# Optimization experiments

Hardware: AMD Instinct MI355X
Metric: run time of the kernel (lower is better)

Reference implementation:

```python
import jax, jax.numpy as jnp
import numpy as np
from jax import lax

IN_CH = 256
NF = 128
B, H, W = 8, 256, 256


def _bn_relu(y, s, b):
    # inference-mode BatchNorm folded into per-channel affine, then ReLU
    return jax.nn.relu(y * s[None, :, None, None] + b[None, :, None, None])


def _upsample_bilinear_ac(x, scale):
    # bilinear upsample, align_corners=True (matches torch nn.Upsample)
    b, c, h, w = x.shape
    Ho, Wo = h * scale, w * scale
    ys = jnp.arange(Ho, dtype=x.dtype) * ((h - 1) / (Ho - 1))
    xs = jnp.arange(Wo, dtype=x.dtype) * ((w - 1) / (Wo - 1))
    y0 = jnp.floor(ys).astype(jnp.int32)
    x0 = jnp.floor(xs).astype(jnp.int32)
    y1 = jnp.minimum(y0 + 1, h - 1)
    x1 = jnp.minimum(x0 + 1, w - 1)
    wy = (ys - y0.astype(x.dtype))[None, None, :, None]
    wx = (xs - x0.astype(x.dtype))[None, None, None, :]
    # interpolate rows then columns
    top = x[:, :, y0, :] * (1 - wy) + x[:, :, y1, :] * wy      # [b,c,Ho,w]
    out = top[:, :, :, x0] * (1 - wx) + top[:, :, :, x1] * wx  # [b,c,Ho,Wo]
    return out


def setup_inputs() -> dict:
    key = jax.random.key(0)
    ks = jax.random.split(key, 6)
    inp = {
        "x": jax.random.normal(ks[0], (B, 64, H, W), dtype=jnp.float32),
        "w1": jax.random.normal(ks[1], (IN_CH, 64, 8, 8), dtype=jnp.float32) * 0.02,
        "bn1_s": jnp.ones((IN_CH,), jnp.float32),
        "bn1_b": jnp.zeros((IN_CH,), jnp.float32),
        "w_fai": jax.random.normal(ks[2], (NF, IN_CH), dtype=jnp.float32) * 0.05,
        "bnf_s": jnp.ones((NF,), jnp.float32),
        "bnf_b": jnp.zeros((NF,), jnp.float32),
        "w_sit": jax.random.normal(ks[3], (NF, IN_CH), dtype=jnp.float32) * 0.05,
        "bns_s": jnp.ones((NF,), jnp.float32),
        "bns_b": jnp.zeros((NF,), jnp.float32),
        "w_gama": jax.random.normal(ks[4], (NF, IN_CH), dtype=jnp.float32) * 0.05,
        "bng_s": jnp.ones((NF,), jnp.float32),
        "bng_b": jnp.zeros((NF,), jnp.float32),
    }
    return inp


def reference(x, w1, bn1_s, bn1_b, w_fai, bnf_s, bnf_b, w_sit, bns_s, bns_b,
              w_gama, bng_s, bng_b):
    # conv1: 8x8 stride-8 conv, BN, ReLU  -> [B, IN_CH, h, w]
    y = lax.conv_general_dilated(x, w1, window_strides=(8, 8), padding="VALID",
                                 dimension_numbers=("NCHW", "OIHW", "NCHW"))
    y = _bn_relu(y, bn1_s, bn1_b)
    b, c, h, w = y.shape
    n = h * w
    # 1x1 conv projections (einsum), BN, ReLU
    fai = _bn_relu(jnp.einsum("bchw,oc->bohw", y, w_fai), bnf_s, bnf_b)
    sit = _bn_relu(jnp.einsum("bchw,oc->bohw", y, w_sit), bns_s, bns_b)
    gama = _bn_relu(jnp.einsum("bchw,oc->bohw", y, w_gama), bng_s, bng_b)
    fai = fai.reshape(b, NF, n)
    sit = sit.reshape(b, NF, n)
    gama = gama.reshape(b, NF, n)
    # non-local attention: sigmoid(fai^T sit) @ gama^T
    sf = jax.nn.sigmoid(jnp.einsum("bcn,bcm->bnm", fai, sit))  # [b, n, n]
    out = jnp.einsum("bnm,bcm->bcn", sf, gama)                  # [b, NF, n]
    out = out.reshape(b, NF, h, w)
    return _upsample_bilinear_ac(out, 8)
```

## Files before the change

### kernel.cpp

```cpp
#include <hip/hip_runtime.h>

typedef __attribute__((ext_vector_type(8))) short short8_t;
typedef __attribute__((ext_vector_type(4))) float float4_t;

__device__ __forceinline__ unsigned short f2bf(float f) {
    unsigned int u = __float_as_uint(f);
    return (unsigned short)((u + 0x7FFFu + ((u >> 16) & 1u)) >> 16);
}
__device__ __forceinline__ unsigned int pkbf(float a, float b) {
    return (unsigned int)f2bf(a) | ((unsigned int)f2bf(b) << 16);
}

__global__ __launch_bounds__(256) void k_wprep(
    const float* __restrict__ w1, unsigned short* __restrict__ w1s)
{
    const int id = blockIdx.x * 256 + threadIdx.x;
    const float4* s = (const float4*)(w1 + id * 8);
    float4 a = s[0], b = s[1];
    int4 o;
    o.x = pkbf(a.x, a.y); o.y = pkbf(a.z, a.w);
    o.z = pkbf(b.x, b.y); o.w = pkbf(b.z, b.w);
    *(int4*)(w1s + id * 8) = o;
}

__global__ __launch_bounds__(512, 2) void k_conv1(
    const float* __restrict__ x, const unsigned short* __restrict__ w1s,
    float* __restrict__ part)
{
    __shared__ unsigned short At[128 * 40];
    __shared__ unsigned short Bt[256 * 40];
    const int tid = threadIdx.x;
    const int mt = blockIdx.x, kc = blockIdx.y;
    const int m0 = mt * 128;
    const int bi = mt >> 3;
    const int oh0 = (mt & 7) * 4;
    const int lane = tid & 63, wid = tid >> 6;
    const int wm = wid & 1, wn = wid >> 1;
    const int quad = lane >> 4, r16 = lane & 15;
    const bool isA = tid < 256;
    const int tA = tid & 255;
    const int rA = tA >> 4, segA = tA & 15;
    const int ohl = rA >> 2, khl = rA & 3;
    const int rowA = ohl * 32 + segA * 2;
    const int koffA = (khl ^ (segA & 3)) * 8;
    const int kbase = kc * 1024;
    float4_t acc[4][4] = {};
    float4 ra[4];
    int4 rb[4];

    if (isA) {
        const int ic = kbase >> 6, kh0 = (kbase >> 3) & 7;
        const int xr = (oh0 + ohl) * 8 + kh0 + khl;
        const float4* s4 = (const float4*)(x + (((bi * 64 + ic) * 256 + xr) * 256 + segA * 16));
        ra[0] = s4[0]; ra[1] = s4[1]; ra[2] = s4[2]; ra[3] = s4[3];
    } else {
        #pragma unroll
        for (int l = 0; l < 4; ++l) {
            const int slot = l * 256 + tA;
            const int row = slot >> 2, p = slot & 3;
            rb[l] = *(const int4*)(w1s + row * 4096 + kbase + p * 8);
        }
    }

    for (int it = 0; it < 32; ++it) {
        if (isA) {
            int4 p0, p1;
            p0.x = pkbf(ra[0].x, ra[0].y); p0.y = pkbf(ra[0].z, ra[0].w);
            p0.z = pkbf(ra[1].x, ra[1].y); p0.w = pkbf(ra[1].z, ra[1].w);
            p1.x = pkbf(ra[2].x, ra[2].y); p1.y = pkbf(ra[2].z, ra[2].w);
            p1.z = pkbf(ra[3].x, ra[3].y); p1.w = pkbf(ra[3].z, ra[3].w);
            *(int4*)&At[rowA * 40 + koffA] = p0;
            *(int4*)&At[(rowA + 1) * 40 + koffA] = p1;
        } else {
            #pragma unroll
            for (int l = 0; l < 4; ++l) {
                const int slot = l * 256 + tA;
                const int row = slot >> 2, p = slot & 3;
                *(int4*)&Bt[row * 40 + p * 8] = rb[l];
            }
        }
        __syncthreads();
        if (it + 1 < 32) {
            const int k0 = kbase + (it + 1) * 32;
            if (isA) {
                const int ic = k0 >> 6, kh0 = (k0 >> 3) & 7;
                const int xr = (oh0 + ohl) * 8 + kh0 + khl;
                const float4* s4 = (const float4*)(x + (((bi * 64 + ic) * 256 + xr) * 256 + segA * 16));
                ra[0] = s4[0]; ra[1] = s4[1]; ra[2] = s4[2]; ra[3] = s4[3];
            } else {
                #pragma unroll
                for (int l = 0; l < 4; ++l) {
                    const int slot = l * 256 + tA;
                    const int row = slot >> 2, p = slot & 3;
                    rb[l] = *(const int4*)(w1s + row * 4096 + k0 + p * 8);
                }
            }
        }
        short8_t aF[4], bF[4];
        #pragma unroll
        for (int i = 0; i < 4; ++i) {
            const int R = wm * 64 + i * 16 + r16;
            aF[i] = *(const short8_t*)&At[R * 40 + (quad ^ ((r16 >> 1) & 3)) * 8];
        }
        #pragma unroll
        for (int j = 0; j < 4; ++j)
            bF[j] = *(const short8_t*)&Bt[(wn * 64 + j * 16 + r16) * 40 + quad * 8];
        #pragma unroll
        for (int i = 0; i < 4; ++i)
            #pragma unroll
            for (int j = 0; j < 4; ++j)
                acc[i][j] = __builtin_amdgcn_mfma_f32_16x16x32_bf16(aF[i], bF[j], acc[i][j], 0, 0, 0);
        __syncthreads();
    }
    float* pp = part + ((size_t)kc << 21);
    #pragma unroll
    for (int i = 0; i < 4; ++i) {
        const int mg = m0 + wm * 64 + i * 16 + quad * 4;
        #pragma unroll
        for (int j = 0; j < 4; ++j) {
            const int ng = wn * 64 + j * 16 + r16;
            #pragma unroll
            for (int r = 0; r < 4; ++r)
                pp[(mg + r) * 256 + ng] = acc[i][j][r];
        }
    }
}

__global__ __launch_bounds__(256, 4) void k_reduce(
    const float* __restrict__ part, const float* __restrict__ s1,
    const float* __restrict__ b1, unsigned short* __restrict__ y)
{
    const int id = blockIdx.x * 256 + threadIdx.x;
    const int c4 = id & 63;
    const float4* p = (const float4*)part + id;
    float4 a = p[0], b = p[524288], c = p[1048576], d = p[1572864];
    float4 s = ((const float4*)s1)[c4], bb = ((const float4*)b1)[c4];
    float vx = fmaxf((a.x + b.x + c.x + d.x) * s.x + bb.x, 0.f);
    float vy = fmaxf((a.y + b.y + c.y + d.y) * s.y + bb.y, 0.f);
    float vz = fmaxf((a.z + b.z + c.z + d.z) * s.z + bb.z, 0.f);
    float vw = fmaxf((a.w + b.w + c.w + d.w) * s.w + bb.w, 0.f);
    int2 o; o.x = pkbf(vx, vy); o.y = pkbf(vz, vw);
    ((int2*)y)[id] = o;
}

__global__ __launch_bounds__(256, 2) void k_proj3(
    const unsigned short* __restrict__ y,
    const float* __restrict__ w_fai, const float* __restrict__ w_sit,
    const float* __restrict__ w_gama,
    const float* __restrict__ fs, const float* __restrict__ fb,
    const float* __restrict__ ss, const float* __restrict__ sb,
    const float* __restrict__ gs, const float* __restrict__ gb,
    unsigned short* __restrict__ P, unsigned short* __restrict__ G)
{
    __shared__ unsigned short At[64 * 40];
    __shared__ unsigned short Bt[64 * 40];
    const int tid = threadIdx.x;
    const int nt = blockIdx.x, mt = blockIdx.y;
    const int m0 = mt * 64;
    const float *W, *S, *Bb;
    if (nt < 2)      { W = w_fai;  S = fs; Bb = fb; }
    else if (nt < 4) { W = w_sit;  S = ss; Bb = sb; }
    else             { W = w_gama; S = gs; Bb = gb; }
    const int roff = (nt * 64) & 127;
    const int lane = tid & 63, wid = tid >> 6;
    const int wm = wid & 1, wn = wid >> 1;
    const int quad = lane >> 4, r16 = lane & 15;
    float4_t acc[2][2] = {};

    for (int k0 = 0; k0 < 256; k0 += 32) {
        {
            const int row = tid >> 2, pp = tid & 3;
            *(int4*)&At[row * 40 + pp * 8] =
                *(const int4*)(y + (m0 + row) * 256 + k0 + pp * 8);
        }
        #pragma unroll
        for (int l = 0; l < 2; ++l) {
            const int slot = l * 256 + tid;
            const int row = slot >> 3, pp = slot & 7;
            float4 v = *(const float4*)(W + (roff + row) * 256 + k0 + pp * 4);
            int2 wv; wv.x = pkbf(v.x, v.y); wv.y = pkbf(v.z, v.w);
            *(int2*)&Bt[row * 40 + pp * 4] = wv;
        }
        __syncthreads();
        short8_t aF[2], bF[2];
        #pragma unroll
        for (int i = 0; i < 2; ++i)
            aF[i] = *(const short8_t*)&At[(wm * 32 + i * 16 + r16) * 40 + quad * 8];
        #pragma unroll
        for (int j = 0; j < 2; ++j)
            bF[j] = *(const short8_t*)&Bt[(wn * 32 + j * 16 + r16) * 40 + quad * 8];
        #pragma unroll
        for (int i = 0; i < 2; ++i)
            #pragma unroll
            for (int j = 0; j < 2; ++j)
                acc[i][j] = __builtin_amdgcn_mfma_f32_16x16x32_bf16(aF[i], bF[j], acc[i][j], 0, 0, 0);
        __syncthreads();
    }
    #pragma unroll
    for (int i = 0; i < 2; ++i) {
        const int mg = m0 + wm * 32 + i * 16 + quad * 4;
        #pragma unroll
        for (int j = 0; j < 2; ++j) {
            const int nl = wn * 32 + j * 16 + r16;
            const float sc = S[roff + nl], bc = Bb[roff + nl];
            if (nt < 4) {
                const int col = nt * 64 + nl;
                #pragma unroll
                for (int r = 0; r < 4; ++r) {
                    float v = fmaxf(acc[i][j][r] * sc + bc, 0.f);
                    P[(mg + r) * 256 + col] = f2bf(v);
                }
            } else {
                const int c = roff + nl;
                #pragma unroll
                for (int r = 0; r < 4; ++r) {
                    float v = fmaxf(acc[i][j][r] * sc + bc, 0.f);
                    const int sp = mg + r;
                    G[((sp >> 10) * 128 + c) * 1024 + (sp & 1023)] = f2bf(v);
                }
            }
        }
    }
}

#define LSTR 152
__global__ __launch_bounds__(256, 2) void k_attn(
    const unsigned short* __restrict__ P, const unsigned short* __restrict__ G,
    float* __restrict__ Opart)
{
    __shared__ unsigned short At[64 * LSTR];
    __shared__ unsigned short Bt[128 * LSTR];
    __shared__ unsigned short Sl[64 * LSTR];
    const int tid = threadIdx.x;
    const int nt = blockIdx.x, zz = blockIdx.y;
    const int b = zz >> 2, kc = zz & 3;
    const int n0 = nt * 64;
    const int base = b * 1024;
    const int lane = tid & 63, wid = tid >> 6;
    const int wm = wid & 1, wn = wid >> 1;
    const int quad = lane >> 4, r16 = lane & 15;
    float4_t acc2[2][4] = {};

    #pragma unroll
    for (int l = 0; l < 4; ++l) {
        const int slot = l * 256 + tid;
        const int row = slot >> 4, p = slot & 15;
        *(int4*)&At[row * LSTR + p * 8] =
            *(const int4*)(P + (base + n0 + row) * 256 + p * 8);
    }
    for (int ms = 0; ms < 2; ++ms) {
        const int m1 = kc * 256 + ms * 128;
        #pragma unroll
        for (int l = 0; l < 8; ++l) {
            const int slot = l * 256 + tid;
            const int row = slot >> 4, p = slot & 15;
            *(int4*)&Bt[row * LSTR + p * 8] =
                *(const int4*)(P + (base + m1 + row) * 256 + 128 + p * 8);
        }
        __syncthreads();
        float4_t acc1[2][4] = {};
        #pragma unroll
        for (int c = 0; c < 4; ++c) {
            short8_t aF[2], bF[4];
            #pragma unroll
            for (int i = 0; i < 2; ++i)
                aF[i] = *(const short8_t*)&At[(wm * 32 + i * 16 + r16) * LSTR + c * 32 + quad * 8];
            #pragma unroll
            for (int j = 0; j < 4; ++j)
                bF[j] = *(const short8_t*)&Bt[(wn * 64 + j * 16 + r16) * LSTR + c * 32 + quad * 8];
            #pragma unroll
            for (int i = 0; i < 2; ++i)
                #pragma unroll
                for (int j = 0; j < 4; ++j)
                    acc1[i][j] = __builtin_amdgcn_mfma_f32_16x16x32_bf16(aF[i], bF[j], acc1[i][j], 0, 0, 0);
        }
        __syncthreads();
        #pragma unroll
        for (int i = 0; i < 2; ++i) {
            const int nl = wm * 32 + i * 16 + quad * 4;
            #pragma unroll
            for (int j = 0; j < 4; ++j) {
                const int ml = wn * 64 + j * 16 + r16;
                #pragma unroll
                for (int r = 0; r < 4; ++r) {
                    const float xv = acc1[i][j][r];
                    const float e = __expf(-xv);
                    const float v = __builtin_amdgcn_rcpf(1.0f + e);
                    Sl[(nl + r) * LSTR + ml] = f2bf(v);
                }
            }
        }
        #pragma unroll
        for (int l = 0; l < 8; ++l) {
            const int slot = l * 256 + tid;
            const int row = slot >> 4, p = slot & 15;
            *(int4*)&Bt[row * LSTR + p * 8] =
                *(const int4*)(G + (b * 128 + row) * 1024 + m1 + p * 8);
        }
        __syncthreads();
        #pragma unroll
        for (int c = 0; c < 4; ++c) {
            short8_t aF[2], bF[4];
            #pragma unroll
            for (int i = 0; i < 2; ++i)
                aF[i] = *(const short8_t*)&Sl[(wm * 32 + i * 16 + r16) * LSTR + c * 32 + quad * 8];
            #pragma unroll
            for (int j = 0; j < 4; ++j)
                bF[j] = *(const short8_t*)&Bt[(wn * 64 + j * 16 + r16) * LSTR + c * 32 + quad * 8];
            #pragma unroll
            for (int i = 0; i < 2; ++i)
                #pragma unroll
                for (int j = 0; j < 4; ++j)
                    acc2[i][j] = __builtin_amdgcn_mfma_f32_16x16x32_bf16(aF[i], bF[j], acc2[i][j], 0, 0, 0);
        }
        __syncthreads();
    }
    float* op = Opart + (size_t)kc * 1048576 + (size_t)b * 131072;
    #pragma unroll
    for (int i = 0; i < 2; ++i) {
        const int nl = n0 + wm * 32 + i * 16 + quad * 4;
        #pragma unroll
        for (int j = 0; j < 4; ++j) {
            const int ch = wn * 64 + j * 16 + r16;
            #pragma unroll
            for (int r = 0; r < 4; ++r)
                op[(nl + r) * 128 + ch] = acc2[i][j][r];
        }
    }
}

__global__ __launch_bounds__(256, 2) void k_up(
    const float* __restrict__ Opart, float* __restrict__ out)
{
    __shared__ float l0[32 * 136];
    __shared__ float l1[32 * 136];
    const int tid = threadIdx.x;
    const int yb = blockIdx.x, b = blockIdx.y;
    const float sc = 31.0f / 255.0f;
    const float fy = yb * sc;
    const int y0 = (int)fy;
    const float wy = fy - (float)y0;
    const int y1 = (y0 + 1 < 32) ? y0 + 1 : 31;
    const float4* r0 = (const float4*)(Opart + (size_t)b * 131072 + y0 * 4096);
    const float4* r1 = (const float4*)(Opart + (size_t)b * 131072 + y1 * 4096);
    #pragma unroll
    for (int j = 0; j < 4; ++j) {
        const int id = j * 256 + tid;
        const int xs = id >> 5, c4 = id & 31;
        float4 a0 = r0[id], a1 = r1[id];
        #pragma unroll
        for (int kc = 1; kc < 4; ++kc) {
            float4 t0 = r0[id + kc * 262144], t1 = r1[id + kc * 262144];
            a0.x += t0.x; a0.y += t0.y; a0.z += t0.z; a0.w += t0.w;
            a1.x += t1.x; a1.y += t1.y; a1.z += t1.z; a1.w += t1.w;
        }
        *(float4*)(l0 + xs * 136 + c4 * 4) = a0;
        *(float4*)(l1 + xs * 136 + c4 * 4) = a1;
    }
    __syncthreads();
    const float fx = tid * sc;
    const int x0 = (int)fx;
    const float wx = fx - (float)x0;
    const int x1 = (x0 + 1 < 32) ? x0 + 1 : 31;
    const float w00 = (1.f - wy) * (1.f - wx), w01 = (1.f - wy) * wx;
    const float w10 = wy * (1.f - wx), w11 = wy * wx;
    const float* a = l0 + x0 * 136;
    const float* bq = l0 + x1 * 136;
    const float* c = l1 + x0 * 136;
    const float* d = l1 + x1 * 136;
    float* op = out + (size_t)b * 8388608 + yb * 256 + tid;
    #pragma unroll 4
    for (int ch = 0; ch < 128; ++ch)
        op[ch * 65536] = w00 * a[ch] + w01 * bq[ch] + w10 * c[ch] + w11 * d[ch];
}

extern "C" void kernel_launch(void* const* d_in, const int* in_sizes, int n_in,
                              void* d_out, int out_size, void* d_ws, size_t ws_size,
                              hipStream_t stream) {
    (void)in_sizes; (void)n_in; (void)out_size; (void)ws_size;
    const float* x      = (const float*)d_in[0];
    const float* w1     = (const float*)d_in[1];
    const float* bn1_s  = (const float*)d_in[2];
    const float* bn1_b  = (const float*)d_in[3];
    const float* w_fai  = (const float*)d_in[4];
    const float* bnf_s  = (const float*)d_in[5];
    const float* bnf_b  = (const float*)d_in[6];
    const float* w_sit  = (const float*)d_in[7];
    const float* bns_s  = (const float*)d_in[8];
    const float* bns_b  = (const float*)d_in[9];
    const float* w_gama = (const float*)d_in[10];
    const float* bng_s  = (const float*)d_in[11];
    const float* bng_b  = (const float*)d_in[12];
    float* out = (float*)d_out;

    char* ws = (char*)d_ws;
    float*          pc    = (float*)ws;
    float*          Opart = (float*)(ws + 16u * 1024 * 1024);
    unsigned short* y     = (unsigned short*)(ws + 32u * 1024 * 1024);
    unsigned short* P     = (unsigned short*)(ws + 36u * 1024 * 1024);
    unsigned short* G     = (unsigned short*)(ws + 40u * 1024 * 1024);
    unsigned short* w1s   = (unsigned short*)(ws + 44u * 1024 * 1024);

    k_wprep <<<dim3(512),      256, 0, stream>>>(w1, w1s);
    k_conv1 <<<dim3(64, 4),    512, 0, stream>>>(x, w1s, pc);
    k_reduce<<<dim3(2048),     256, 0, stream>>>(pc, bn1_s, bn1_b, y);
    k_proj3 <<<dim3(6, 128),   256, 0, stream>>>(y, w_fai, w_sit, w_gama,
                                                 bnf_s, bnf_b, bns_s, bns_b,
                                                 bng_s, bng_b, P, G);
    k_attn  <<<dim3(16, 32),   256, 0, stream>>>(P, G, Opart);
    k_up    <<<dim3(256, 8),   256, 0, stream>>>(Opart, out);
}
```

Baseline: 472.8 us.

## Deepen register prefetch in conv1 and prefetch attention tiles into registers

In the conv kernel, the k-loop is unrolled by two and uses two register buffers, so global loads are issued two stages ahead of their shared-memory commit. In the attention kernel, the sit tile and the gama tile are loaded into registers before the preceding MFMA phase and stored to shared memory afterwards, which lets global latency overlap compute instead of stalling before each barrier. This raises register pressure, which could cut occupancy or cause spills under the launch bounds, and the conv loop gains an extra barrier per iteration.

```diff
diff --git a/kernel.cpp b/kernel.cpp
--- a/kernel.cpp
+++ b/kernel.cpp
@@ -21,6 +21,54 @@
     o.x = pkbf(a.x, a.y); o.y = pkbf(a.z, a.w);
     o.z = pkbf(b.x, b.y); o.w = pkbf(b.z, b.w);
     *(int4*)(w1s + id * 8) = o;
+}
+
+#define CONV_LOAD_A(dst, k0q) {                                               \
+    const int ic = (k0q) >> 6, kh0 = ((k0q) >> 3) & 7;                        \
+    const int xr = (oh0 + ohl) * 8 + kh0 + khl;                               \
+    const float4* s4 = (const float4*)(x + (((bi * 64 + ic) * 256 + xr) * 256 + segA * 16)); \
+    dst[0] = s4[0]; dst[1] = s4[1]; dst[2] = s4[2]; dst[3] = s4[3];           \
+}
+#define CONV_LOAD_B(dst, k0q) {                                               \
+    _Pragma("unroll")                                                         \
+    for (int l = 0; l < 4; ++l) {                                             \
+        const int slot = l * 256 + tA;                                        \
+        const int row = slot >> 2, p = slot & 3;                              \
+        dst[l] = *(const int4*)(w1s + row * 4096 + (k0q) + p * 8);            \
+    }                                                                         \
+}
+#define CONV_COMMIT_A(src) {                                                  \
+    int4 p0, p1;                                                              \
+    p0.x = pkbf(src[0].x, src[0].y); p0.y = pkbf(src[0].z, src[0].w);         \
+    p0.z = pkbf(src[1].x, src[1].y); p0.w = pkbf(src[1].z, src[1].w);         \
+    p1.x = pkbf(src[2].x, src[2].y); p1.y = pkbf(src[2].z, src[2].w);         \
+    p1.z = pkbf(src[3].x, src[3].y); p1.w = pkbf(src[3].z, src[3].w);         \
+    *(int4*)&At[rowA * 40 + koffA] = p0;                                      \
+    *(int4*)&At[(rowA + 1) * 40 + koffA] = p1;                                \
+}
+#define CONV_COMMIT_B(src) {                                                  \
+    _Pragma("unroll")                                                         \
+    for (int l = 0; l < 4; ++l) {                                             \
+        const int slot = l * 256 + tA;                                        \
+        const int row = slot >> 2, p = slot & 3;                              \
+        *(int4*)&Bt[row * 40 + p * 8] = src[l];                               \
+    }                                                                         \
+}
+#define CONV_MFMA() {                                                         \
+    short8_t aF[4], bF[4];                                                    \
+    _Pragma("unroll")                                                         \
+    for (int i = 0; i < 4; ++i) {                                             \
+        const int R = wm * 64 + i * 16 + r16;                                 \
+        aF[i] = *(const short8_t*)&At[R * 40 + (quad ^ ((r16 >> 1) & 3)) * 8];\
+    }                                                                         \
+    _Pragma("unroll")                                                         \
+    for (int j = 0; j < 4; ++j)                                               \
+        bF[j] = *(const short8_t*)&Bt[(wn * 64 + j * 16 + r16) * 40 + quad * 8]; \
+    _Pragma("unroll")                                                         \
+    for (int i = 0; i < 4; ++i)                                               \
+        _Pragma("unroll")                                                     \
+        for (int j = 0; j < 4; ++j)                                           \
+            acc[i][j] = __builtin_amdgcn_mfma_f32_16x16x32_bf16(aF[i], bF[j], acc[i][j], 0, 0, 0); \
 }
 
 __global__ __launch_bounds__(512, 2) void k_conv1(
@@ -45,71 +93,28 @@
     const int koffA = (khl ^ (segA & 3)) * 8;
     const int kbase = kc * 1024;
     float4_t acc[4][4] = {};
-    float4 ra[4];
-    int4 rb[4];
-
-    if (isA) {
-        const int ic = kbase >> 6, kh0 = (kbase >> 3) & 7;
-        const int xr = (oh0 + ohl) * 8 + kh0 + khl;
-        const float4* s4 = (const float4*)(x + (((bi * 64 + ic) * 256 + xr) * 256 + segA * 16));
-        ra[0] = s4[0]; ra[1] = s4[1]; ra[2] = s4[2]; ra[3] = s4[3];
-    } else {
-        #pragma unroll
-        for (int l = 0; l < 4; ++l) {
-            const int slot = l * 256 + tA;
-            const int row = slot >> 2, p = slot & 3;
-            rb[l] = *(const int4*)(w1s + row * 4096 + kbase + p * 8);
-        }
-    }
-
-    for (int it = 0; it < 32; ++it) {
-        if (isA) {
-            int4 p0, p1;
-            p0.x = pkbf(ra[0].x, ra[0].y); p0.y = pkbf(ra[0].z, ra[0].w);
-            p0.z = pkbf(ra[1].x, ra[1].y); p0.w = pkbf(ra[1].z, ra[1].w);
-            p1.x = pkbf(ra[2].x, ra[2].y); p1.y = pkbf(ra[2].z, ra[2].w);
-            p1.z = pkbf(ra[3].x, ra[3].y); p1.w = pkbf(ra[3].z, ra[3].w);
-            *(int4*)&At[rowA * 40 + koffA] = p0;
-            *(int4*)&At[(rowA + 1) * 40 + koffA] = p1;
-        } else {
-            #pragma unroll
-            for (int l = 0; l < 4; ++l) {
-                const int slot = l * 256 + tA;
-                const int row = slot >> 2, p = slot & 3;
-                *(int4*)&Bt[row * 40 + p * 8] = rb[l];
-            }
-        }
-        __syncthreads();
-        if (it + 1 < 32) {
-            const int k0 = kbase + (it + 1) * 32;
-            if (isA) {
-                const int ic = k0 >> 6, kh0 = (k0 >> 3) & 7;
-                const int xr = (oh0 + ohl) * 8 + kh0 + khl;
-                const float4* s4 = (const float4*)(x + (((bi * 64 + ic) * 256 + xr) * 256 + segA * 16));
-                ra[0] = s4[0]; ra[1] = s4[1]; ra[2] = s4[2]; ra[3] = s4[3];
-            } else {
-                #pragma unroll
-                for (int l = 0; l < 4; ++l) {
-                    const int slot = l * 256 + tA;
-                    const int row = slot >> 2, p = slot & 3;
-                    rb[l] = *(const int4*)(w1s + row * 4096 + k0 + p * 8);
-                }
-            }
-        }
-        short8_t aF[4], bF[4];
-        #pragma unroll
-        for (int i = 0; i < 4; ++i) {
-            const int R = wm * 64 + i * 16 + r16;
-            aF[i] = *(const short8_t*)&At[R * 40 + (quad ^ ((r16 >> 1) & 3)) * 8];
-        }
-        #pragma unroll
-        for (int j = 0; j < 4; ++j)
-            bF[j] = *(const short8_t*)&Bt[(wn * 64 + j * 16 + r16) * 40 + quad * 8];
-        #pragma unroll
-        for (int i = 0; i < 4; ++i)
-            #pragma unroll
-            for (int j = 0; j < 4; ++j)
-                acc[i][j] = __builtin_amdgcn_mfma_f32_16x16x32_bf16(aF[i], bF[j], acc[i][j], 0, 0, 0);
+    float4 raA[4], raB[4];
+    int4 rbA[4], rbB[4];
+
+    if (isA) { CONV_LOAD_A(raA, kbase); CONV_LOAD_A(raB, kbase + 32); }
+    else     { CONV_LOAD_B(rbA, kbase); CONV_LOAD_B(rbB, kbase + 32); }
+
+    for (int it = 0; it < 32; it += 2) {
+        if (isA) CONV_COMMIT_A(raA) else CONV_COMMIT_B(rbA);
+        __syncthreads();
+        if (it + 2 < 32) {
+            const int k0 = kbase + (it + 2) * 32;
+            if (isA) CONV_LOAD_A(raA, k0) else CONV_LOAD_B(rbA, k0);
+        }
+        CONV_MFMA();
+        __syncthreads();
+        if (isA) CONV_COMMIT_A(raB) else CONV_COMMIT_B(rbB);
+        __syncthreads();
+        if (it + 3 < 32) {
+            const int k0 = kbase + (it + 3) * 32;
+            if (isA) CONV_LOAD_A(raB, k0) else CONV_LOAD_B(rbB, k0);
+        }
+        CONV_MFMA();
         __syncthreads();
     }
     float* pp = part + ((size_t)kc << 21);
@@ -239,7 +244,9 @@
     const int lane = tid & 63, wid = tid >> 6;
     const int wm = wid & 1, wn = wid >> 1;
     const int quad = lane >> 4, r16 = lane & 15;
+    const int srow = tid >> 4, sp16 = tid & 15;
     float4_t acc2[2][4] = {};
+    int4 rs[8], rg[8];
 
     #pragma unroll
     for (int l = 0; l < 4; ++l) {
@@ -248,16 +255,22 @@
         *(int4*)&At[row * LSTR + p * 8] =
             *(const int4*)(P + (base + n0 + row) * 256 + p * 8);
     }
+    {
+        const int m1 = kc * 256;
+        #pragma unroll
+        for (int l = 0; l < 8; ++l)
+            rs[l] = *(const int4*)(P + (base + m1 + (l * 16 + srow)) * 256 + 128 + sp16 * 8);
+    }
+    #pragma unroll
     for (int ms = 0; ms < 2; ++ms) {
         const int m1 = kc * 256 + ms * 128;
         #pragma unroll
-        for (int l = 0; l < 8; ++l) {
-            const int slot = l * 256 + tid;
-            const int row = slot >> 4, p = slot & 15;
-            *(int4*)&Bt[row * LSTR + p * 8] =
-                *(const int4*)(P + (base + m1 + row) * 256 + 128 + p * 8);
-        }
-        __syncthreads();
+        for (int l = 0; l < 8; ++l)
+            *(int4*)&Bt[(l * 16 + srow) * LSTR + sp16 * 8] = rs[l];
+        __syncthreads();
+        #pragma unroll
+        for (int l = 0; l < 8; ++l)
+            rg[l] = *(const int4*)(G + (b * 128 + (l * 16 + srow)) * 1024 + m1 + sp16 * 8);
         float4_t acc1[2][4] = {};
         #pragma unroll
         for (int c = 0; c < 4; ++c) {
@@ -291,11 +304,13 @@
             }
         }
         #pragma unroll
-        for (int l = 0; l < 8; ++l) {
-            const int slot = l * 256 + tid;
-            const int row = slot >> 4, p = slot & 15;
-            *(int4*)&Bt[row * LSTR + p * 8] =
-                *(const int4*)(G + (b * 128 + row) * 1024 + m1 + p * 8);
+        for (int l = 0; l < 8; ++l)
+            *(int4*)&Bt[(l * 16 + srow) * LSTR + sp16 * 8] = rg[l];
+        if (ms == 0) {
+            const int m1n = kc * 256 + 128;
+            #pragma unroll
+            for (int l = 0; l < 8; ++l)
+                rs[l] = *(const int4*)(P + (base + m1n + (l * 16 + srow)) * 256 + 128 + sp16 * 8);
         }
         __syncthreads();
         #pragma unroll
```

Result: slower. 509.6 us (+7.8%).
